# Optimization experiments

Measured on AMD Instinct MI355X. Metric: run time of the kernel, lower is better.

Reference implementation:

```python
import jax, jax.numpy as jnp
import numpy as np

N_HEADS = 64
N_KV = 8
HEAD_DIM = 128
HIDDEN = 8192
BATCH = 32
PAD_LEN = 2048  # nearest_32(start_pos + 1) with start_pos = 2047


def setup_inputs() -> dict:
    key = jax.random.key(0)
    ks = jax.random.split(key, 8)
    w = 0.02
    return {
        "x": jax.random.normal(ks[0], (BATCH, 1, HIDDEN), jnp.float32),
        "wq": jax.random.normal(ks[1], (HIDDEN, N_HEADS * HEAD_DIM), jnp.float32) * w,
        "wk": jax.random.normal(ks[2], (HIDDEN, N_KV * HEAD_DIM), jnp.float32) * w,
        "wv": jax.random.normal(ks[3], (HIDDEN, N_KV * HEAD_DIM), jnp.float32) * w,
        "wo": jax.random.normal(ks[4], (N_HEADS * HEAD_DIM, HIDDEN), jnp.float32) * w,
        "rot_mat": jax.random.normal(ks[5], (HEAD_DIM, HEAD_DIM), jnp.float32) * w,
        "k_cache": jax.random.normal(ks[6], (BATCH, N_KV, PAD_LEN, HEAD_DIM), jnp.float32),
        "v_cache": jax.random.normal(ks[7], (BATCH, N_KV, PAD_LEN, HEAD_DIM), jnp.float32),
        "start_pos": 2047,
    }


def reference(x, wq, wk, wv, wo, rot_mat, k_cache, v_cache, start_pos):
    B = x.shape[0]
    L = k_cache.shape[2]  # padded past length (nearest_32(start_pos+1))
    scale = 1.0 / np.sqrt(HEAD_DIM).astype(np.float32)

    xt = x[:, 0]  # [B, HIDDEN], seq_len == 1 (decode)
    # QKV projections + rotary applied via explicit matmul with rot_mat
    q = (xt @ wq).reshape(B, N_HEADS, HEAD_DIM) @ rot_mat      # [B, nH, d]
    k_new = (xt @ wk).reshape(B, N_KV, HEAD_DIM) @ rot_mat     # [B, nKV, d]
    v_new = (xt @ wv).reshape(B, N_KV, HEAD_DIM)               # [B, nKV, d]

    # in-place KV cache update at current position
    keys = k_cache.at[:, :, start_pos].set(k_new)              # [B, nKV, L, d]
    vals = v_cache.at[:, :, start_pos].set(v_new)

    # grouped (multi-query) attention: 8 q-heads per kv-head
    qg = q.reshape(B, N_KV, N_HEADS // N_KV, HEAD_DIM)         # [B, nKV, g, d]
    scores = jnp.einsum("bkgd,bkld->bkgl", qg, keys) * scale   # [B, nKV, g, L]
    # padded causal mask: positions beyond start_pos are masked with finfo.min
    mask = jnp.where(jnp.arange(L) > start_pos,
                     jnp.finfo(scores.dtype).min, 0.0).astype(scores.dtype)
    attn = jax.nn.softmax(scores + mask, axis=-1)
    out = jnp.einsum("bkgl,bkld->bkgd", attn, vals)            # [B, nKV, g, d]
    out = out.reshape(B, N_HEADS * HEAD_DIM) @ wo              # dense out-proj
    return out[:, None, :]                                     # [B, 1, HIDDEN]
```

## Files before the change

kernel.cpp:

```cpp
#include <hip/hip_runtime.h>
#include <hip/hip_bf16.h>

#define HIDDEN 8192
#define NHEADS 64
#define NKV 8
#define HD 128
#define BATCH 32
#define PADLEN 2048
#define NCHUNK 4
#define CHUNKLEN 512

using bf16x8 = __attribute__((ext_vector_type(8))) short;
using f32x4 = __attribute__((ext_vector_type(4))) float;

__device__ __forceinline__ void gld16(const float* g, float* l) {
    __builtin_amdgcn_global_load_lds(
        (const __attribute__((address_space(1))) void*)g,
        (__attribute__((address_space(3))) void*)l,
        16, 0, 0);
}

__device__ __forceinline__ float readlane_f(float v, int lane) {
    return __uint_as_float(__builtin_amdgcn_readlane(__float_as_uint(v), lane));
}

__device__ __forceinline__ short f2bf(float f) {
    unsigned u = __float_as_uint(f);
    u += 0x7fff + ((u >> 16) & 1);
    return (short)(u >> 16);
}
__device__ __forceinline__ float bf2f(short s) {
    return __uint_as_float(((unsigned)(unsigned short)s) << 16);
}

__global__ __launch_bounds__(256) void cvt_split(const float* __restrict__ in,
                                                 short* __restrict__ hi,
                                                 short* __restrict__ lo, int n4) {
    int i = blockIdx.x * 256 + threadIdx.x;
    if (i >= n4) return;
    float4 v = ((const float4*)in)[i];
    short4 h, l;
    h.x = f2bf(v.x); l.x = f2bf(v.x - bf2f(h.x));
    h.y = f2bf(v.y); l.y = f2bf(v.y - bf2f(h.y));
    h.z = f2bf(v.z); l.z = f2bf(v.z - bf2f(h.z));
    h.w = f2bf(v.w); l.w = f2bf(v.w - bf2f(h.w));
    ((short4*)hi)[i] = h;
    ((short4*)lo)[i] = l;
}

#define QSEC 262144
#define KSEC 294912
#define QKV_STRIDE 327680
#define NSPLIT 16
#define KSLICE 512

__global__ __launch_bounds__(256) void gemm_mfma(
        const short* __restrict__ xhi, const short* __restrict__ xlo,
        const float* __restrict__ W0, const float* __restrict__ W1,
        const float* __restrict__ W2, float* __restrict__ P, size_t pstride) {
    const int tid = threadIdx.x;
    const int wv = tid >> 6, ln = tid & 63;
    const int cb = blockIdx.x, kb = blockIdx.y;

    const float* W; int N2; size_t so; int nbase;
    if (cb < 64)      { W = W0; N2 = 8192; so = 0;    nbase = cb * 128; }
    else if (cb < 72) { W = W1; N2 = 1024; so = QSEC; nbase = (cb - 64) * 128; }
    else              { W = W2; N2 = 1024; so = KSEC; nbase = (cb - 72) * 128; }

    const int n0 = nbase + wv * 32;
    const int lrow = ln & 15;
    const int kgrp = ln >> 4;
    const int k0 = kb * KSLICE;

    const float* wp0 = W + (size_t)(k0 + kgrp * 8) * N2 + (n0 + lrow);
    const float* wp1 = wp0 + 16;
    const short* xh0 = xhi + (size_t)lrow * HIDDEN + k0 + kgrp * 8;
    const short* xl0 = xlo + (size_t)lrow * HIDDEN + k0 + kgrp * 8;
    const short* xh1 = xh0 + (size_t)16 * HIDDEN;
    const short* xl1 = xl0 + (size_t)16 * HIDDEN;

    f32x4 acc00 = {0.f,0.f,0.f,0.f}, acc01 = {0.f,0.f,0.f,0.f};
    f32x4 acc10 = {0.f,0.f,0.f,0.f}, acc11 = {0.f,0.f,0.f,0.f};

    float c0[8], c1[8], d0[8], d1[8], e0[8], e1[8];
    bf16x8 A0h, A0l, A1h, A1l, N0h, N0l, N1h, N1l;

    auto loadB = [&](int kk, float (&b0)[8], float (&b1)[8]) {
#pragma unroll
        for (int j = 0; j < 8; ++j) {
            b0[j] = wp0[(size_t)(kk + j) * N2];
            b1[j] = wp1[(size_t)(kk + j) * N2];
        }
    };
    auto loadA = [&](int kk, bf16x8& h0, bf16x8& l0, bf16x8& h1, bf16x8& l1) {
        h0 = *(const bf16x8*)(xh0 + kk);
        l0 = *(const bf16x8*)(xl0 + kk);
        h1 = *(const bf16x8*)(xh1 + kk);
        l1 = *(const bf16x8*)(xl1 + kk);
    };
    auto domfma = [&](float (&b0)[8], float (&b1)[8],
                      bf16x8 ah0, bf16x8 al0, bf16x8 ah1, bf16x8 al1) {
        bf16x8 bh0, bl0, bh1, bl1;
#pragma unroll
        for (int j = 0; j < 8; ++j) {
            short h0 = f2bf(b0[j]); bh0[j] = h0; bl0[j] = f2bf(b0[j] - bf2f(h0));
            short h1 = f2bf(b1[j]); bh1[j] = h1; bl1[j] = f2bf(b1[j] - bf2f(h1));
        }
        acc00 = __builtin_amdgcn_mfma_f32_16x16x32_bf16(ah0, bh0, acc00, 0, 0, 0);
        acc10 = __builtin_amdgcn_mfma_f32_16x16x32_bf16(ah1, bh0, acc10, 0, 0, 0);
        acc01 = __builtin_amdgcn_mfma_f32_16x16x32_bf16(ah0, bh1, acc01, 0, 0, 0);
        acc11 = __builtin_amdgcn_mfma_f32_16x16x32_bf16(ah1, bh1, acc11, 0, 0, 0);
        acc00 = __builtin_amdgcn_mfma_f32_16x16x32_bf16(al0, bh0, acc00, 0, 0, 0);
        acc10 = __builtin_amdgcn_mfma_f32_16x16x32_bf16(al1, bh0, acc10, 0, 0, 0);
        acc01 = __builtin_amdgcn_mfma_f32_16x16x32_bf16(al0, bh1, acc01, 0, 0, 0);
        acc11 = __builtin_amdgcn_mfma_f32_16x16x32_bf16(al1, bh1, acc11, 0, 0, 0);
        acc00 = __builtin_amdgcn_mfma_f32_16x16x32_bf16(ah0, bl0, acc00, 0, 0, 0);
        acc10 = __builtin_amdgcn_mfma_f32_16x16x32_bf16(ah1, bl0, acc10, 0, 0, 0);
        acc01 = __builtin_amdgcn_mfma_f32_16x16x32_bf16(ah0, bl1, acc01, 0, 0, 0);
        acc11 = __builtin_amdgcn_mfma_f32_16x16x32_bf16(ah1, bl1, acc11, 0, 0, 0);
    };

    loadB(0, c0, c1);
    loadA(0, A0h, A0l, A1h, A1l);
    loadB(32, d0, d1);
#pragma unroll
    for (int kk = 0; kk < KSLICE - 64; kk += 32) {
        loadB(kk + 64, e0, e1);
        loadA(kk + 32, N0h, N0l, N1h, N1l);
        domfma(c0, c1, A0h, A0l, A1h, A1l);
#pragma unroll
        for (int j = 0; j < 8; ++j) {
            c0[j] = d0[j]; c1[j] = d1[j];
            d0[j] = e0[j]; d1[j] = e1[j];
        }
        A0h = N0h; A0l = N0l; A1h = N1h; A1l = N1l;
    }
    loadA(KSLICE - 32, N0h, N0l, N1h, N1l);
    domfma(c0, c1, A0h, A0l, A1h, A1l);
    domfma(d0, d1, N0h, N0l, N1h, N1l);

    float* pb = P + (size_t)kb * pstride + so;
#pragma unroll
    for (int r = 0; r < 4; ++r) {
        int row0 = kgrp * 4 + r;
        pb[(size_t)row0 * N2 + n0 + lrow]             = acc00[r];
        pb[(size_t)row0 * N2 + n0 + 16 + lrow]        = acc01[r];
        pb[(size_t)(row0 + 16) * N2 + n0 + lrow]      = acc10[r];
        pb[(size_t)(row0 + 16) * N2 + n0 + 16 + lrow] = acc11[r];
    }
}

__global__ __launch_bounds__(256) void reduce_split(const float* __restrict__ P,
                                                    float* __restrict__ out,
                                                    int nelem, size_t pstride) {
    int i = (blockIdx.x * 256 + threadIdx.x) * 4;
    if (i >= nelem) return;
    float4 a = *(const float4*)(P + i);
#pragma unroll 4
    for (int s = 1; s < NSPLIT; ++s) {
        float4 b = *(const float4*)(P + (size_t)s * pstride + i);
        a.x += b.x; a.y += b.y; a.z += b.z; a.w += b.w;
    }
    *(float4*)(out + i) = a;
}

#define RROWS 16
__global__ __launch_bounds__(128) void reduce_rotary(const float* __restrict__ P,
                                                     const float* __restrict__ rot,
                                                     float* __restrict__ qout,
                                                     float* __restrict__ kout,
                                                     float* __restrict__ vout) {
    __shared__ float rows[RROWS][HD];
    const int tid = threadIdx.x;
    const int blk = blockIdx.x;

    if (blk < 144) {
        const int row0 = blk * RROWS;
        for (int i = tid; i < RROWS * HD; i += 128) {
            int r = row0 + (i >> 7);
            int d = i & 127;
            size_t off;
            if (r < BATCH * NHEADS) off = (size_t)(r >> 6) * 8192 + (r & 63) * 128 + d;
            else {
                int r2 = r - BATCH * NHEADS;
                off = QSEC + (size_t)(r2 >> 3) * 1024 + (r2 & 7) * 128 + d;
            }
            float a = P[off];
#pragma unroll 5
            for (int s = 1; s < NSPLIT; ++s) a += P[(size_t)s * QKV_STRIDE + off];
            rows[i >> 7][d] = a;
        }
        __syncthreads();

        float acc[RROWS];
#pragma unroll
        for (int r = 0; r < RROWS; ++r) acc[r] = 0.f;
        for (int d4 = 0; d4 < HD; d4 += 4) {
            float r0 = rot[(size_t)(d4 + 0) * HD + tid];
            float r1 = rot[(size_t)(d4 + 1) * HD + tid];
            float r2 = rot[(size_t)(d4 + 2) * HD + tid];
            float r3 = rot[(size_t)(d4 + 3) * HD + tid];
#pragma unroll
            for (int r = 0; r < RROWS; ++r) {
                float4 xv = *(const float4*)&rows[r][d4];
                acc[r] = fmaf(xv.x, r0, acc[r]);
                acc[r] = fmaf(xv.y, r1, acc[r]);
                acc[r] = fmaf(xv.z, r2, acc[r]);
                acc[r] = fmaf(xv.w, r3, acc[r]);
            }
        }
#pragma unroll
        for (int r = 0; r < RROWS; ++r) {
            int gr = row0 + r;
            float* dst = (gr < BATCH * NHEADS)
                             ? (qout + (size_t)gr * HD)
                             : (kout + (size_t)(gr - BATCH * NHEADS) * HD);
            dst[tid] = acc[r];
        }
    } else {
        const int row0 = (blk - 144) * RROWS;
        for (int i = tid; i < RROWS * HD; i += 128) {
            int r2 = row0 + (i >> 7);
            int d = i & 127;
            size_t off = KSEC + (size_t)(r2 >> 3) * 1024 + (r2 & 7) * 128 + d;
            float a = P[off];
#pragma unroll 5
            for (int s = 1; s < NSPLIT; ++s) a += P[(size_t)s * QKV_STRIDE + off];
            vout[(size_t)r2 * HD + d] = a;
        }
    }
}

#define TILE 16
#define NBUF 4
__global__ __launch_bounds__(512, 4) void attn_decode(
        const float* __restrict__ qr, const float* __restrict__ kr,
        const float* __restrict__ vnew, const float* __restrict__ kcache,
        const float* __restrict__ vcache, const int* __restrict__ sp_ptr,
        float* __restrict__ part_acc, float* __restrict__ part_md) {
    __shared__ float4 kt[NBUF][TILE][32];
    __shared__ float4 vt[NBUF][TILE][32];

    const int tid = threadIdx.x;
    const int wv = tid >> 6, ln = tid & 63;
    const int row = ln & 15, qd = ln >> 4;
    const int dslot = ln & 31, hh = ln >> 5;
    const int chunk = blockIdx.x >> 8;
    const int b  = (blockIdx.x >> 3) & 31;
    const int kv = blockIdx.x & 7;
    const int chunk0 = chunk * CHUNKLEN;
    const int sp = sp_ptr[0];
    const float scale = 0.08838834764831845f;
    const int bh = b * NHEADS + kv * 8 + wv;

    const float* kbase = kcache + (size_t)(b * NKV + kv) * PADLEN * HD;
    const float* vbase = vcache + (size_t)(b * NKV + kv) * PADLEN * HD;
    const float* knew  = kr   + (size_t)(b * NKV + kv) * HD;
    const float* vnw   = vnew + (size_t)(b * NKV + kv) * HD;

    float4 qreg[8];
    {
        const float4* qsrc = (const float4*)(qr + (size_t)bh * HD) + qd * 8;
#pragma unroll
        for (int i = 0; i < 8; ++i) qreg[i] = qsrc[i];
    }

    const int sr  = wv * 2 + (ln >> 5);
    const int sj  = ln & 31;
    const int sjk = sj ^ (sr & 7);

    float m_run = -1e30f, dsum = 0.f;
    float4 acc = make_float4(0.f, 0.f, 0.f, 0.f);

    int valid = sp + 1 - chunk0;
    int nt = valid <= 0 ? 0 : (valid + TILE - 1) >> 4;
    if (nt > CHUNKLEN / TILE) nt = CHUNKLEN / TILE;

    auto stage = [&](int ts, int slot) {
        const int gl = chunk0 + (ts << 4) + sr;
        const float* krow = (gl == sp) ? knew : (kbase + (size_t)gl * HD);
        const float* vrow = (gl == sp) ? vnw  : (vbase + (size_t)gl * HD);
        gld16(krow + (sjk << 2), (float*)&kt[slot][0][0] + wv * 256);
        gld16(vrow + (sj  << 2), (float*)&vt[slot][0][0] + wv * 256);
    };

    auto compute = [&](int t) {
        const float4 (*kt_)[32] = kt[t & 3];
        const float4 (*vt_)[32] = vt[t & 3];
        float sh = 0.f;
#pragma unroll
        for (int jj = 0; jj < 8; ++jj) {
            float4 kk = kt_[row][(qd * 8 + jj) ^ (row & 7)];
            float4 qq = qreg[jj];
            sh = fmaf(qq.x, kk.x, sh);
            sh = fmaf(qq.y, kk.y, sh);
            sh = fmaf(qq.z, kk.z, sh);
            sh = fmaf(qq.w, kk.w, sh);
        }
        sh += __shfl_xor(sh, 16);
        sh += __shfl_xor(sh, 32);
        float s0 = sh * scale;
        const int l0 = chunk0 + (t << 4) + row;
        const bool dead = l0 > sp;
        if (dead) s0 = -1e30f;

        float mt = s0;
        mt = fmaxf(mt, __shfl_xor(mt, 1));
        mt = fmaxf(mt, __shfl_xor(mt, 2));
        mt = fmaxf(mt, __shfl_xor(mt, 4));
        mt = fmaxf(mt, __shfl_xor(mt, 8));
        float mnew = fmaxf(m_run, mt);
        float f = __expf(m_run - mnew);
        float p0 = dead ? 0.f : __expf(s0 - mnew);
        m_run = mnew;
        dsum = dsum * f + p0;
        acc.x *= f; acc.y *= f; acc.z *= f; acc.w *= f;

#pragma unroll
        for (int i = 0; i < 8; ++i) {
            float4 vv = vt_[hh * 8 + i][dslot];
            float pa = readlane_f(p0, i);
            float pb = readlane_f(p0, 8 + i);
            float pr = hh ? pb : pa;
            acc.x = fmaf(pr, vv.x, acc.x);
            acc.y = fmaf(pr, vv.y, acc.y);
            acc.z = fmaf(pr, vv.z, acc.z);
            acc.w = fmaf(pr, vv.w, acc.w);
        }
    };

    if (nt > 0) {
        stage(0, 0);
        stage(nt > 1 ? 1 : 0, 1);
        for (int t = 0; t < nt; ++t) {
            int ts = t + 2 < nt ? t + 2 : nt - 1;
            stage(ts, (t + 2) & 3);
            asm volatile("s_waitcnt vmcnt(4)" ::: "memory");
            __builtin_amdgcn_s_barrier();
            compute(t);
        }
    }

    acc.x += __shfl_xor(acc.x, 32);
    acc.y += __shfl_xor(acc.y, 32);
    acc.z += __shfl_xor(acc.z, 32);
    acc.w += __shfl_xor(acc.w, 32);
    float dd = dsum;
    dd += __shfl_xor(dd, 1);
    dd += __shfl_xor(dd, 2);
    dd += __shfl_xor(dd, 4);
    dd += __shfl_xor(dd, 8);

    if (hh == 0)
        *(float4*)(part_acc + ((size_t)chunk * (BATCH * NHEADS) + bh) * HD + dslot * 4) = acc;
    if (ln == 0) {
        float2 md = make_float2(m_run, dd);
        *(float2*)(part_md + ((size_t)chunk * (BATCH * NHEADS) + bh) * 2) = md;
    }
}

__global__ __launch_bounds__(128) void attn_combine_cvt(
        const float* __restrict__ part_acc, const float* __restrict__ part_md,
        short* __restrict__ ahi, short* __restrict__ alo) {
    const int bh = blockIdx.x;
    const int d = threadIdx.x;
    float m[NCHUNK], dd[NCHUNK];
    float M = -1e30f;
#pragma unroll
    for (int c = 0; c < NCHUNK; ++c) {
        m[c]  = part_md[((size_t)c * (BATCH * NHEADS) + bh) * 2];
        dd[c] = part_md[((size_t)c * (BATCH * NHEADS) + bh) * 2 + 1];
        M = fmaxf(M, m[c]);
    }
    float D = 0.f, o = 0.f;
#pragma unroll
    for (int c = 0; c < NCHUNK; ++c) {
        float w = __expf(m[c] - M);
        D += dd[c] * w;
        o += part_acc[((size_t)c * (BATCH * NHEADS) + bh) * HD + d] * w;
    }
    float v = o / D;
    short h = f2bf(v);
    ahi[(size_t)bh * HD + d] = h;
    alo[(size_t)bh * HD + d] = f2bf(v - bf2f(h));
}

extern "C" void kernel_launch(void* const* d_in, const int* in_sizes, int n_in,
                              void* d_out, int out_size, void* d_ws, size_t ws_size,
                              hipStream_t stream) {
    const float* x   = (const float*)d_in[0];
    const float* wq  = (const float*)d_in[1];
    const float* wk  = (const float*)d_in[2];
    const float* wv  = (const float*)d_in[3];
    const float* wo  = (const float*)d_in[4];
    const float* rot = (const float*)d_in[5];
    const float* kc  = (const float*)d_in[6];
    const float* vc  = (const float*)d_in[7];
    const int*   sp  = (const int*)d_in[8];
    float* out = (float*)d_out;

    float* ws = (float*)d_ws;
    float* v_buf    = ws;
    float* qr_buf   = ws + 327680;
    float* kr_buf   = ws + 589824;
    short* xhi      = (short*)(ws + 884736);
    short* xlo      = (short*)(ws + 884736 + 131072);
    short* ahi      = (short*)(ws + 884736 + 262144);
    short* alo      = (short*)(ws + 884736 + 393216);
    float* P        = ws + 884736 + 524288;
    float* part_acc = P;
    float* part_md  = P + 1048576;

    cvt_split<<<(QSEC / 4 + 255) / 256, 256, 0, stream>>>(x, xhi, xlo, QSEC / 4);
    gemm_mfma<<<dim3(80, NSPLIT), 256, 0, stream>>>(xhi, xlo, wq, wk, wv, P, QKV_STRIDE);
    reduce_rotary<<<160, 128, 0, stream>>>(P, rot, qr_buf, kr_buf, v_buf);

    attn_decode<<<NCHUNK * BATCH * NKV, 512, 0, stream>>>(
        qr_buf, kr_buf, v_buf, kc, vc, sp, part_acc, part_md);
    attn_combine_cvt<<<BATCH * NHEADS, 128, 0, stream>>>(part_acc, part_md, ahi, alo);

    gemm_mfma<<<dim3(64, NSPLIT), 256, 0, stream>>>(ahi, alo, wo, wo, wo, P, QSEC);
    reduce_split<<<(QSEC / 4 + 255) / 256, 256, 0, stream>>>(P, out, QSEC, QSEC);
}
```

Measured before the change: 314.2 us.

## Halve GEMM column tile, drop manual prefetch, double attention chunks

The split-bf16 GEMM now gives each wave 16 output columns instead of 32, which doubles the grid to 160 and 128 column blocks. The three-stage software prefetch of weights is replaced by a plain unrolled loop, and launch bounds now request 6 waves per SIMD so the lower register use can turn into more resident waves. Attention decode uses 8 chunks of 256 instead of 4 of 512, doubling the attention blocks, and the partial-result buffer offset moves to make room. The aim is to hide memory latency through more parallel work rather than explicit pipelining. The risks are that A-operand loads are repeated across twice as many blocks and that the combine step has more partials to merge.

```diff
diff --git a/kernel.cpp b/kernel.cpp
--- a/kernel.cpp
+++ b/kernel.cpp
@@ -7,8 +7,8 @@
 #define HD 128
 #define BATCH 32
 #define PADLEN 2048
-#define NCHUNK 4
-#define CHUNKLEN 512
+#define NCHUNK 8
+#define CHUNKLEN 256
 
 using bf16x8 = __attribute__((ext_vector_type(8))) short;
 using f32x4 = __attribute__((ext_vector_type(4))) float;
@@ -54,7 +54,7 @@
 #define NSPLIT 16
 #define KSLICE 512
 
-__global__ __launch_bounds__(256) void gemm_mfma(
+__global__ __launch_bounds__(256, 6) void gemm_mfma(
         const short* __restrict__ xhi, const short* __restrict__ xlo,
         const float* __restrict__ W0, const float* __restrict__ W1,
         const float* __restrict__ W2, float* __restrict__ P, size_t pstride) {
@@ -63,90 +63,54 @@
     const int cb = blockIdx.x, kb = blockIdx.y;
 
     const float* W; int N2; size_t so; int nbase;
-    if (cb < 64)      { W = W0; N2 = 8192; so = 0;    nbase = cb * 128; }
-    else if (cb < 72) { W = W1; N2 = 1024; so = QSEC; nbase = (cb - 64) * 128; }
-    else              { W = W2; N2 = 1024; so = KSEC; nbase = (cb - 72) * 128; }
-
-    const int n0 = nbase + wv * 32;
+    if (cb < 128)      { W = W0; N2 = 8192; so = 0;    nbase = cb * 64; }
+    else if (cb < 144) { W = W1; N2 = 1024; so = QSEC; nbase = (cb - 128) * 64; }
+    else               { W = W2; N2 = 1024; so = KSEC; nbase = (cb - 144) * 64; }
+
+    const int n0 = nbase + wv * 16;
     const int lrow = ln & 15;
     const int kgrp = ln >> 4;
     const int k0 = kb * KSLICE;
 
-    const float* wp0 = W + (size_t)(k0 + kgrp * 8) * N2 + (n0 + lrow);
-    const float* wp1 = wp0 + 16;
+    const float* wp = W + (size_t)(k0 + kgrp * 8) * N2 + (n0 + lrow);
     const short* xh0 = xhi + (size_t)lrow * HIDDEN + k0 + kgrp * 8;
     const short* xl0 = xlo + (size_t)lrow * HIDDEN + k0 + kgrp * 8;
     const short* xh1 = xh0 + (size_t)16 * HIDDEN;
     const short* xl1 = xl0 + (size_t)16 * HIDDEN;
 
-    f32x4 acc00 = {0.f,0.f,0.f,0.f}, acc01 = {0.f,0.f,0.f,0.f};
-    f32x4 acc10 = {0.f,0.f,0.f,0.f}, acc11 = {0.f,0.f,0.f,0.f};
-
-    float c0[8], c1[8], d0[8], d1[8], e0[8], e1[8];
-    bf16x8 A0h, A0l, A1h, A1l, N0h, N0l, N1h, N1l;
-
-    auto loadB = [&](int kk, float (&b0)[8], float (&b1)[8]) {
+    f32x4 acc0 = {0.f,0.f,0.f,0.f}, acc1 = {0.f,0.f,0.f,0.f};
+
+#pragma unroll
+    for (int kk = 0; kk < KSLICE; kk += 32) {
+        float b[8];
+#pragma unroll
+        for (int j = 0; j < 8; ++j) b[j] = wp[(size_t)(kk + j) * N2];
+        bf16x8 a0h = *(const bf16x8*)(xh0 + kk);
+        bf16x8 a0l = *(const bf16x8*)(xl0 + kk);
+        bf16x8 a1h = *(const bf16x8*)(xh1 + kk);
+        bf16x8 a1l = *(const bf16x8*)(xl1 + kk);
+
+        bf16x8 bh, bl;
 #pragma unroll
         for (int j = 0; j < 8; ++j) {
-            b0[j] = wp0[(size_t)(kk + j) * N2];
-            b1[j] = wp1[(size_t)(kk + j) * N2];
-        }
-    };
-    auto loadA = [&](int kk, bf16x8& h0, bf16x8& l0, bf16x8& h1, bf16x8& l1) {
-        h0 = *(const bf16x8*)(xh0 + kk);
-        l0 = *(const bf16x8*)(xl0 + kk);
-        h1 = *(const bf16x8*)(xh1 + kk);
-        l1 = *(const bf16x8*)(xl1 + kk);
-    };
-    auto domfma = [&](float (&b0)[8], float (&b1)[8],
-                      bf16x8 ah0, bf16x8 al0, bf16x8 ah1, bf16x8 al1) {
-        bf16x8 bh0, bl0, bh1, bl1;
-#pragma unroll
-        for (int j = 0; j < 8; ++j) {
-            short h0 = f2bf(b0[j]); bh0[j] = h0; bl0[j] = f2bf(b0[j] - bf2f(h0));
-            short h1 = f2bf(b1[j]); bh1[j] = h1; bl1[j] = f2bf(b1[j] - bf2f(h1));
-        }
-        acc00 = __builtin_amdgcn_mfma_f32_16x16x32_bf16(ah0, bh0, acc00, 0, 0, 0);
-        acc10 = __builtin_amdgcn_mfma_f32_16x16x32_bf16(ah1, bh0, acc10, 0, 0, 0);
-        acc01 = __builtin_amdgcn_mfma_f32_16x16x32_bf16(ah0, bh1, acc01, 0, 0, 0);
-        acc11 = __builtin_amdgcn_mfma_f32_16x16x32_bf16(ah1, bh1, acc11, 0, 0, 0);
-        acc00 = __builtin_amdgcn_mfma_f32_16x16x32_bf16(al0, bh0, acc00, 0, 0, 0);
-        acc10 = __builtin_amdgcn_mfma_f32_16x16x32_bf16(al1, bh0, acc10, 0, 0, 0);
-        acc01 = __builtin_amdgcn_mfma_f32_16x16x32_bf16(al0, bh1, acc01, 0, 0, 0);
-        acc11 = __builtin_amdgcn_mfma_f32_16x16x32_bf16(al1, bh1, acc11, 0, 0, 0);
-        acc00 = __builtin_amdgcn_mfma_f32_16x16x32_bf16(ah0, bl0, acc00, 0, 0, 0);
-        acc10 = __builtin_amdgcn_mfma_f32_16x16x32_bf16(ah1, bl0, acc10, 0, 0, 0);
-        acc01 = __builtin_amdgcn_mfma_f32_16x16x32_bf16(ah0, bl1, acc01, 0, 0, 0);
-        acc11 = __builtin_amdgcn_mfma_f32_16x16x32_bf16(ah1, bl1, acc11, 0, 0, 0);
-    };
-
-    loadB(0, c0, c1);
-    loadA(0, A0h, A0l, A1h, A1l);
-    loadB(32, d0, d1);
-#pragma unroll
-    for (int kk = 0; kk < KSLICE - 64; kk += 32) {
-        loadB(kk + 64, e0, e1);
-        loadA(kk + 32, N0h, N0l, N1h, N1l);
-        domfma(c0, c1, A0h, A0l, A1h, A1l);
-#pragma unroll
-        for (int j = 0; j < 8; ++j) {
-            c0[j] = d0[j]; c1[j] = d1[j];
-            d0[j] = e0[j]; d1[j] = e1[j];
-        }
-        A0h = N0h; A0l = N0l; A1h = N1h; A1l = N1l;
-    }
-    loadA(KSLICE - 32, N0h, N0l, N1h, N1l);
-    domfma(c0, c1, A0h, A0l, A1h, A1l);
-    domfma(d0, d1, N0h, N0l, N1h, N1l);
+            short h = f2bf(b[j]);
+            bh[j] = h;
+            bl[j] = f2bf(b[j] - bf2f(h));
+        }
+        acc0 = __builtin_amdgcn_mfma_f32_16x16x32_bf16(a0h, bh, acc0, 0, 0, 0);
+        acc1 = __builtin_amdgcn_mfma_f32_16x16x32_bf16(a1h, bh, acc1, 0, 0, 0);
+        acc0 = __builtin_amdgcn_mfma_f32_16x16x32_bf16(a0l, bh, acc0, 0, 0, 0);
+        acc1 = __builtin_amdgcn_mfma_f32_16x16x32_bf16(a1l, bh, acc1, 0, 0, 0);
+        acc0 = __builtin_amdgcn_mfma_f32_16x16x32_bf16(a0h, bl, acc0, 0, 0, 0);
+        acc1 = __builtin_amdgcn_mfma_f32_16x16x32_bf16(a1h, bl, acc1, 0, 0, 0);
+    }
 
     float* pb = P + (size_t)kb * pstride + so;
 #pragma unroll
     for (int r = 0; r < 4; ++r) {
-        int row0 = kgrp * 4 + r;
-        pb[(size_t)row0 * N2 + n0 + lrow]             = acc00[r];
-        pb[(size_t)row0 * N2 + n0 + 16 + lrow]        = acc01[r];
-        pb[(size_t)(row0 + 16) * N2 + n0 + lrow]      = acc10[r];
-        pb[(size_t)(row0 + 16) * N2 + n0 + 16 + lrow] = acc11[r];
+        int row = kgrp * 4 + r;
+        pb[(size_t)row * N2 + n0 + lrow]        = acc0[r];
+        pb[(size_t)(row + 16) * N2 + n0 + lrow] = acc1[r];
     }
 }
 
@@ -409,16 +373,16 @@
     short* alo      = (short*)(ws + 884736 + 393216);
     float* P        = ws + 884736 + 524288;
     float* part_acc = P;
-    float* part_md  = P + 1048576;
+    float* part_md  = P + 2097152;
 
     cvt_split<<<(QSEC / 4 + 255) / 256, 256, 0, stream>>>(x, xhi, xlo, QSEC / 4);
-    gemm_mfma<<<dim3(80, NSPLIT), 256, 0, stream>>>(xhi, xlo, wq, wk, wv, P, QKV_STRIDE);
+    gemm_mfma<<<dim3(160, NSPLIT), 256, 0, stream>>>(xhi, xlo, wq, wk, wv, P, QKV_STRIDE);
     reduce_rotary<<<160, 128, 0, stream>>>(P, rot, qr_buf, kr_buf, v_buf);
 
     attn_decode<<<NCHUNK * BATCH * NKV, 512, 0, stream>>>(
         qr_buf, kr_buf, v_buf, kc, vc, sp, part_acc, part_md);
     attn_combine_cvt<<<BATCH * NHEADS, 128, 0, stream>>>(part_acc, part_md, ahi, alo);
 
-    gemm_mfma<<<dim3(64, NSPLIT), 256, 0, stream>>>(ahi, alo, wo, wo, wo, P, QSEC);
+    gemm_mfma<<<dim3(128, NSPLIT), 256, 0, stream>>>(ahi, alo, wo, wo, wo, P, QSEC);
     reduce_split<<<(QSEC / 4 + 255) / 256, 256, 0, stream>>>(P, out, QSEC, QSEC);
 }
```

Measured after the change: 401.4 us. +27.8%, slower.

## Split attention into more KV chunks and simplify GEMM prefetch to double buffering

Applied to the files above, without the earlier changes.

Raises the number of sequence chunks per (batch, kv-head) in decode attention from 4 to 8 so more blocks run in parallel, and moves the partial max/denominator buffer to make room for the larger partial accumulator. Replaces the triple-buffered register prefetch in the MFMA GEMM with a two-stage ping-pong and adds a minimum-blocks hint to launch bounds to cap register use and raise occupancy. The trade-offs are more partial results for the combine step to merge, and less load-ahead depth in the GEMM.

```diff
diff --git a/kernel.cpp b/kernel.cpp
--- a/kernel.cpp
+++ b/kernel.cpp
@@ -7,8 +7,8 @@
 #define HD 128
 #define BATCH 32
 #define PADLEN 2048
-#define NCHUNK 4
-#define CHUNKLEN 512
+#define NCHUNK 8
+#define CHUNKLEN 256
 
 using bf16x8 = __attribute__((ext_vector_type(8))) short;
 using f32x4 = __attribute__((ext_vector_type(4))) float;
@@ -54,7 +54,7 @@
 #define NSPLIT 16
 #define KSLICE 512
 
-__global__ __launch_bounds__(256) void gemm_mfma(
+__global__ __launch_bounds__(256, 4) void gemm_mfma(
         const short* __restrict__ xhi, const short* __restrict__ xlo,
         const float* __restrict__ W0, const float* __restrict__ W1,
         const float* __restrict__ W2, float* __restrict__ P, size_t pstride) {
@@ -82,8 +82,8 @@
     f32x4 acc00 = {0.f,0.f,0.f,0.f}, acc01 = {0.f,0.f,0.f,0.f};
     f32x4 acc10 = {0.f,0.f,0.f,0.f}, acc11 = {0.f,0.f,0.f,0.f};
 
-    float c0[8], c1[8], d0[8], d1[8], e0[8], e1[8];
-    bf16x8 A0h, A0l, A1h, A1l, N0h, N0l, N1h, N1l;
+    float cB0[8], cB1[8], dB0[8], dB1[8];
+    bf16x8 cA0h, cA0l, cA1h, cA1l, dA0h, dA0l, dA1h, dA1l;
 
     auto loadB = [&](int kk, float (&b0)[8], float (&b1)[8]) {
 #pragma unroll
@@ -120,33 +120,28 @@
         acc11 = __builtin_amdgcn_mfma_f32_16x16x32_bf16(ah1, bl1, acc11, 0, 0, 0);
     };
 
-    loadB(0, c0, c1);
-    loadA(0, A0h, A0l, A1h, A1l);
-    loadB(32, d0, d1);
-#pragma unroll
-    for (int kk = 0; kk < KSLICE - 64; kk += 32) {
-        loadB(kk + 64, e0, e1);
-        loadA(kk + 32, N0h, N0l, N1h, N1l);
-        domfma(c0, c1, A0h, A0l, A1h, A1l);
-#pragma unroll
-        for (int j = 0; j < 8; ++j) {
-            c0[j] = d0[j]; c1[j] = d1[j];
-            d0[j] = e0[j]; d1[j] = e1[j];
-        }
-        A0h = N0h; A0l = N0l; A1h = N1h; A1l = N1l;
-    }
-    loadA(KSLICE - 32, N0h, N0l, N1h, N1l);
-    domfma(c0, c1, A0h, A0l, A1h, A1l);
-    domfma(d0, d1, N0h, N0l, N1h, N1l);
+    loadB(0, cB0, cB1);
+    loadA(0, cA0h, cA0l, cA1h, cA1l);
+#pragma unroll
+    for (int kk = 0; kk < KSLICE; kk += 64) {
+        loadB(kk + 32, dB0, dB1);
+        loadA(kk + 32, dA0h, dA0l, dA1h, dA1l);
+        domfma(cB0, cB1, cA0h, cA0l, cA1h, cA1l);
+        if (kk + 64 < KSLICE) {
+            loadB(kk + 64, cB0, cB1);
+            loadA(kk + 64, cA0h, cA0l, cA1h, cA1l);
+        }
+        domfma(dB0, dB1, dA0h, dA0l, dA1h, dA1l);
+    }
 
     float* pb = P + (size_t)kb * pstride + so;
 #pragma unroll
     for (int r = 0; r < 4; ++r) {
-        int row0 = kgrp * 4 + r;
-        pb[(size_t)row0 * N2 + n0 + lrow]             = acc00[r];
-        pb[(size_t)row0 * N2 + n0 + 16 + lrow]        = acc01[r];
-        pb[(size_t)(row0 + 16) * N2 + n0 + lrow]      = acc10[r];
-        pb[(size_t)(row0 + 16) * N2 + n0 + 16 + lrow] = acc11[r];
+        int row = kgrp * 4 + r;
+        pb[(size_t)row * N2 + n0 + lrow]              = acc00[r];
+        pb[(size_t)row * N2 + n0 + 16 + lrow]         = acc01[r];
+        pb[(size_t)(row + 16) * N2 + n0 + lrow]       = acc10[r];
+        pb[(size_t)(row + 16) * N2 + n0 + 16 + lrow]  = acc11[r];
     }
 }
 
@@ -409,7 +404,7 @@
     short* alo      = (short*)(ws + 884736 + 393216);
     float* P        = ws + 884736 + 524288;
     float* part_acc = P;
-    float* part_md  = P + 1048576;
+    float* part_md  = P + 2097152;
 
     cvt_split<<<(QSEC / 4 + 255) / 256, 256, 0, stream>>>(x, xhi, xlo, QSEC / 4);
     gemm_mfma<<<dim3(80, NSPLIT), 256, 0, stream>>>(xhi, xlo, wq, wk, wv, P, QKV_STRIDE);
```

Result: slower. 341.7 us (+8.8%).
